# Performance work log

Hardware: AMD Instinct MI355X
Metric: run time of the kernel (lower is better)

Reference implementation:

```python
import jax, jax.numpy as jnp
import numpy as np

# Model dims (match init_kwargs): dim=768, num_heads=12, num_kv_heads=2 -> G=6, head_dim=64
DIM, HKV, G, D = 768, 2, 6, 64


def setup_inputs() -> dict:
    key = jax.random.key(0)
    ks = jax.random.split(key, 9)
    w = 0.02  # init scale for weights
    return {
        "x": jax.random.normal(ks[0], (8, 1024, DIM), dtype=jnp.float32),
        "depth_k": jax.random.normal(ks[1], (8, 1024, HKV, D), dtype=jnp.float32),
        "depth_v": jax.random.normal(ks[2], (8, 1024, HKV, D), dtype=jnp.float32),
        "Wq": jax.random.normal(ks[3], (DIM, DIM), dtype=jnp.float32) * w,
        "bq": jnp.zeros((DIM,), dtype=jnp.float32),
        "Wkv": jax.random.normal(ks[4], (2 * HKV * D, DIM), dtype=jnp.float32) * w,
        "bkv": jnp.zeros((2 * HKV * D,), dtype=jnp.float32),
        "Wproj": jax.random.normal(ks[5], (DIM, DIM), dtype=jnp.float32) * w,
        "bproj": jnp.zeros((DIM,), dtype=jnp.float32),
    }


def reference(x, depth_k, depth_v, Wq, bq, Wkv, bkv, Wproj, bproj):
    B, N, C = x.shape
    scale = D ** -0.5
    # Q projection, GQA groups unfolded into the sequence dim: [B, N*G, Hkv, D]
    q = (x @ Wq.T + bq).reshape(B, N * G, HKV, D)
    # KV projection: [B, N, 2, Hkv, D]
    kv = (x @ Wkv.T + bkv).reshape(B, N, 2, HKV, D)
    k, v = kv[:, :, 0], kv[:, :, 1]
    # Concatenate depth (previous-layer) KV cache along the sequence dim
    k_full = jnp.concatenate([depth_k, k], axis=1)  # [B, N_cache+N, Hkv, D]
    v_full = jnp.concatenate([depth_v, v], axis=1)
    # Full (non-causal) attention per kv head over the unfolded query sequence
    scores = jnp.einsum('bqhd,bkhd->bhqk', q, k_full) * scale  # [B, Hkv, N*G, Kv]
    attn = jax.nn.softmax(scores, axis=-1)
    o = jnp.einsum('bhqk,bkhd->bqhd', attn, v_full)  # [B, N*G, Hkv, D]
    out = o.reshape(B, N, C) @ Wproj.T + bproj  # fold G*Hkv*D back to C=dim
    return out, k, v
```

## Files before the change

### kernel.cpp

```cpp
#include <hip/hip_runtime.h>

using sh8 = __attribute__((ext_vector_type(8))) short;
using sh4 = __attribute__((ext_vector_type(4))) short;
using fx4 = __attribute__((ext_vector_type(4))) float;

#define MFMA(a,b,c)   __builtin_amdgcn_mfma_f32_16x16x32_bf16((a),(b),(c),0,0,0)

__device__ __forceinline__ short f2bf(float f) {
    union { float f; unsigned u; } v; v.f = f;
    return (short)((v.u + 0x7fffu + ((v.u >> 16) & 1u)) >> 16);
}

__device__ __forceinline__ unsigned cvtpk(float lo, float hi) {
    unsigned r;
    asm("v_cvt_pk_bf16_f32 %0, %1, %2" : "=v"(r) : "v"(lo), "v"(hi));
    return r;
}

__device__ __forceinline__ sh8 pack8(float4 a, float4 b) {
    union { unsigned u[4]; sh8 s; } r;
    r.u[0] = cvtpk(a.x, a.y);
    r.u[1] = cvtpk(a.z, a.w);
    r.u[2] = cvtpk(b.x, b.y);
    r.u[3] = cvtpk(b.z, b.w);
    return r.s;
}

#define QSCALE 0.18033688011112042f

#define GLOAD_LDS16(gsrc, ldst) __builtin_amdgcn_global_load_lds( \
    (const __attribute__((address_space(1))) void*)(gsrc),        \
    (__attribute__((address_space(3))) void*)(ldst), 16, 0, 0)

__global__ __launch_bounds__(256) void cast_k(const float* __restrict__ x,
                                              const float* __restrict__ Wq,
                                              const float* __restrict__ Wkv,
                                              short* __restrict__ xbf,
                                              short* __restrict__ wqbf,
                                              short* __restrict__ wkvbf)
{
    const int blk = blockIdx.x, t = threadIdx.x;
    const float* src; short* dst; size_t idx8;
    if (blk < 3072)      { src = x;   dst = xbf;   idx8 = ((size_t)blk * 256 + t) * 8; }
    else if (blk < 3360) { src = Wq;  dst = wqbf;  idx8 = ((size_t)(blk - 3072) * 256 + t) * 8; }
    else                 { src = Wkv; dst = wkvbf; idx8 = ((size_t)(blk - 3360) * 256 + t) * 8; }
    float4 a = *(const float4*)(src + idx8);
    float4 b = *(const float4*)(src + idx8 + 4);
    *(sh8*)&dst[idx8] = pack8(a, b);
}

__global__ __launch_bounds__(256) void wpcast_k(const float* __restrict__ Wp,
                                                short* __restrict__ wpbf)
{
    const size_t idx8 = ((size_t)blockIdx.x * 256 + threadIdx.x) * 8;
    float4 a = *(const float4*)(Wp + idx8);
    float4 b = *(const float4*)(Wp + idx8 + 4);
    *(sh8*)&wpbf[idx8] = pack8(a, b);
}


__global__ __launch_bounds__(256) void prep_k(const short* __restrict__ xbf,
                                              const short* __restrict__ wqbf,
                                              const short* __restrict__ wkvbf,
                                              const float* __restrict__ bq,
                                              const float* __restrict__ bkv,
                                              const float* __restrict__ dk,
                                              const float* __restrict__ dv,
                                              float* __restrict__ ok,
                                              float* __restrict__ ov,
                                              short* __restrict__ q_ws,
                                              short* __restrict__ k_ws,
                                              short* __restrict__ vT_ws)
{
    __shared__ alignas(16) short L[4][16][512];
    const int blk = blockIdx.x;
    const int t   = threadIdx.x;

    if (blk < 512) {
        const int x8 = blk & 7, jj = blk >> 3;
        const int m  = x8 * 8 + (jj >> 3);
        const int nn = jj & 7;
        const bool isq = (nn < 6);
        const int  bm  = m * 128, bn = (isq ? nn : nn - 6) * 128;
        const short* Wmat = isq ? wqbf : wkvbf;

        const int wave = t >> 6, lane = t & 63;
        const int wm   = wave >> 1, wn = wave & 1;
        const int lhi  = lane >> 4, llo = lane & 15;
        const int l15  = lane & 15, l4 = lane >> 4;

        const short* aSrc0 = xbf  + (size_t)(bm + wave*16     + l15)*768 + l4*8;
        const short* aSrc1 = xbf  + (size_t)(bm + (wave+4)*16 + l15)*768 + l4*8;
        const short* bSrc0 = Wmat + (size_t)(bn + wave*16     + l15)*768 + l4*8;
        const short* bSrc1 = Wmat + (size_t)(bn + (wave+4)*16 + l15)*768 + l4*8;

        auto stage = [&](int s) {
            const int r = s & 3;
            GLOAD_LDS16(aSrc0 + s*32, &L[r][wave][0]);
            GLOAD_LDS16(aSrc1 + s*32, &L[r][4 + wave][0]);
            GLOAD_LDS16(bSrc0 + s*32, &L[r][8 + wave][0]);
            GLOAD_LDS16(bSrc1 + s*32, &L[r][12 + wave][0]);
        };

        fx4 zero = {0.f, 0.f, 0.f, 0.f};
        fx4 acc[4][4];
        #pragma unroll
        for (int a = 0; a < 4; ++a)
            #pragma unroll
            for (int b2 = 0; b2 < 4; ++b2) acc[a][b2] = zero;

        stage(0);
        stage(1);

        for (int s = 0; s < 24; ++s) {
            if (s < 22) {
                stage(s + 2);
                asm volatile("s_waitcnt vmcnt(8)" ::: "memory");
            } else if (s == 22) {
                asm volatile("s_waitcnt vmcnt(4)" ::: "memory");
            } else {
                asm volatile("s_waitcnt vmcnt(0)" ::: "memory");
            }
            __builtin_amdgcn_s_barrier();
            __builtin_amdgcn_sched_barrier(0);

            const short* Lb = (const short*)&L[s & 3][0][0];
            const int lo = lane * 8;
            sh8 af[4], bf[4];
            #pragma unroll
            for (int mt = 0; mt < 4; ++mt)
                af[mt] = *(const sh8*)(Lb + (wm*4 + mt)*512 + lo);
            #pragma unroll
            for (int nt = 0; nt < 4; ++nt)
                bf[nt] = *(const sh8*)(Lb + (8 + wn*4 + nt)*512 + lo);
            #pragma unroll
            for (int mt = 0; mt < 4; ++mt)
                #pragma unroll
                for (int nt = 0; nt < 4; ++nt)
                    acc[mt][nt] = MFMA(af[mt], bf[nt], acc[mt][nt]);
        }

        if (isq) {
            #pragma unroll
            for (int nt = 0; nt < 4; ++nt) {
                const int c = bn + wn*64 + nt*16 + llo;
                const float bias = bq[c];
                const int g = c >> 7, h = (c >> 6) & 1, d = c & 63;
                #pragma unroll
                for (int mt = 0; mt < 4; ++mt) {
                    const int m0 = bm + wm*64 + mt*16 + lhi*4;
                    #pragma unroll
                    for (int r = 0; r < 4; ++r) {
                        const int mr = m0 + r;
                        const int b = mr >> 10, n = mr & 1023;
                        const float val = (acc[mt][nt][r] + bias) * QSCALE;
                        q_ws[((size_t)(b*2 + h)*6144 + n*6 + g)*64 + d] = f2bf(val);
                    }
                }
            }
        } else {
            #pragma unroll
            for (int nt = 0; nt < 4; ++nt) {
                const int c = bn + wn*64 + nt*16 + llo;
                const float bias = bkv[c];
                const int s = c >> 7, h = (c >> 6) & 1, d = c & 63;
                #pragma unroll
                for (int mt = 0; mt < 4; ++mt) {
                    const int m0 = bm + wm*64 + mt*16 + lhi*4;
                    const int b = m0 >> 10, n0 = m0 & 1023;
                    float vals[4];
                    #pragma unroll
                    for (int r = 0; r < 4; ++r) vals[r] = acc[mt][nt][r] + bias;
                    const int key = 1024 + n0;
                    if (s == 0) {
                        #pragma unroll
                        for (int r = 0; r < 4; ++r)
                            ok[((size_t)(b*1024 + n0 + r)*2 + h)*64 + d] = vals[r];
                        const int kb_ = key >> 6, nt_ = (key >> 4) & 3;
                        const int half = d >> 5, lhiK = (d >> 3) & 3, jK = d & 7;
                        const size_t base = (size_t)(b*2 + h)*131072
                            + (size_t)(((((kb_*4 + nt_)*2 + half)*64) + lhiK*16 + (key & 15))*8 + jK);
                        #pragma unroll
                        for (int r = 0; r < 4; ++r)
                            k_ws[base + r*8] = f2bf(vals[r]);
                    } else {
                        #pragma unroll
                        for (int r = 0; r < 4; ++r)
                            ov[((size_t)(b*1024 + n0 + r)*2 + h)*64 + d] = vals[r];
                        const int kb_ = key >> 6, g_ = (key >> 5) & 1, k5 = key & 31;
                        const int half5 = k5 >> 4, lhi5 = (k5 >> 2) & 3;
                        const int dt_ = d >> 4, llov = d & 15;
                        short4 pk = make_short4(f2bf(vals[0]), f2bf(vals[1]),
                                                f2bf(vals[2]), f2bf(vals[3]));
                        const size_t base = (size_t)(b*2 + h)*131072
                            + (size_t)(((((kb_*2 + g_)*4 + dt_)*64) + lhi5*16 + llov)*8 + half5*4);
                        *(short4*)&vT_ws[base] = pk;
                    }
                }
            }
        }
    } else if (blk < 1536) {
        const size_t idx4 = ((size_t)(blk - 512) * 256 + t) * 4;
        const int b  = (int)(idx4 >> 17);
        const int rm = (int)(idx4 & 131071);
        const int tt = rm >> 7, h = (rm >> 6) & 1, d = rm & 63;
        float4 v = *(const float4*)(dk + idx4);
        short4 pk = make_short4(f2bf(v.x), f2bf(v.y), f2bf(v.z), f2bf(v.w));
        const int kb_ = tt >> 6, nt_ = (tt >> 4) & 3, lloK = tt & 15;
        const int half = d >> 5, lhiK = (d >> 3) & 3, jK = d & 7;
        const size_t addr = (size_t)(b*2 + h)*131072
            + (size_t)(((((kb_*4 + nt_)*2 + half)*64) + lhiK*16 + lloK)*8 + jK);
        *(short4*)&k_ws[addr] = pk;
    } else {
        const int unit = (blk - 1536)*4 + (t >> 6);
        const int lane = t & 63, lhi = lane >> 4, llo = lane & 15;
        const int dt_ = unit & 3, g_ = (unit >> 2) & 1;
        const int kb_ = (unit >> 3) & 15, bh = unit >> 7;
        const int b = bh >> 1, h = bh & 1;
        const float* s0 = dv
            + ((size_t)((b*1024 + kb_*64 + g_*32 + lhi*4)*2 + h))*64 + dt_*16 + llo;
        union { short s[8]; sh8 v8; } o;
        #pragma unroll
        for (int jv = 0; jv < 4; ++jv) o.s[jv]     = f2bf(s0[(size_t)jv * 128]);
        #pragma unroll
        for (int jv = 0; jv < 4; ++jv) o.s[4 + jv] = f2bf(s0[(size_t)(16 + jv) * 128]);
        *(sh8*)&vT_ws[((size_t)bh*256 + (kb_*2 + g_)*4 + dt_)*512 + lane*8] = o.v8;
    }
}

__global__ __launch_bounds__(256) void attn_k(const short* __restrict__ q_ws,
                                              const short* __restrict__ k_ws,
                                              const short* __restrict__ vT_ws,
                                              short* __restrict__ o_ws)
{
    __shared__ alignas(16) short L[4][8][512];
    const int t    = threadIdx.x;
    const int wave = t >> 6, lane = t & 63;
    const int lhi  = lane >> 4, llo = lane & 15;
    const int blk  = blockIdx.x;
    const int x8   = blk & 7, jj = blk >> 3;
    const int bh   = x8 * 2 + (jj >= 48 ? 1 : 0);
    const int qt   = (jj >= 48) ? (jj - 48) : jj;
    const int b    = bh >> 1, h = bh & 1;

    const short* qb = q_ws + ((size_t)bh*6144 + qt*128 + wave*32) * 64;
    sh8 qf[2][2];
    #pragma unroll
    for (int s = 0; s < 2; ++s) {
        qf[s][0] = *(const sh8*)(qb + (s*16 + llo)*64 + lhi*8);
        qf[s][1] = *(const sh8*)(qb + (s*16 + llo)*64 + lhi*8 + 32);
    }

    const short* kbase = k_ws  + (size_t)bh*131072;
    const short* vbase = vT_ws + (size_t)bh*131072;

    fx4 zero = {0.f, 0.f, 0.f, 0.f};
    fx4 oacc[2][4];
    fx4 lacc[2];
    #pragma unroll
    for (int s = 0; s < 2; ++s) {
        lacc[s] = zero;
        #pragma unroll
        for (int dt = 0; dt < 4; ++dt) oacc[s][dt] = zero;
    }

    union { unsigned u[4]; sh8 s8; } onesu;
    onesu.u[0] = onesu.u[1] = onesu.u[2] = onesu.u[3] = 0x3F803F80u;
    const sh8 ones = onesu.s8;

    auto stage = [&](int g) {
        const short* ks = kbase + ((size_t)g*4 + wave)*512 + lane*8;
        const short* vs = vbase + ((size_t)g*4 + wave)*512 + lane*8;
        GLOAD_LDS16(ks, &L[g & 3][wave][0]);
        GLOAD_LDS16(vs, &L[g & 3][4 + wave][0]);
    };

    stage(0);
    stage(1);

    for (int g = 0; g < 64; ++g) {
        if (g < 62) {
            stage(g + 2);
            asm volatile("s_waitcnt vmcnt(4)" ::: "memory");
        } else if (g == 62) {
            asm volatile("s_waitcnt vmcnt(2)" ::: "memory");
        } else {
            asm volatile("s_waitcnt vmcnt(0)" ::: "memory");
        }
        __builtin_amdgcn_s_barrier();
        __builtin_amdgcn_sched_barrier(0);

        const short* Lb = (const short*)&L[g & 3][0][0];
        const int lo = lane * 8;
        sh8 K0 = *(const sh8*)(Lb + lo);
        sh8 K1 = *(const sh8*)(Lb + 512  + lo);
        sh8 K2 = *(const sh8*)(Lb + 1024 + lo);
        sh8 K3 = *(const sh8*)(Lb + 1536 + lo);
        sh8 V0 = *(const sh8*)(Lb + 2048 + lo);
        sh8 V1 = *(const sh8*)(Lb + 2560 + lo);
        sh8 V2 = *(const sh8*)(Lb + 3072 + lo);
        sh8 V3 = *(const sh8*)(Lb + 3584 + lo);

        #pragma unroll
        for (int s = 0; s < 2; ++s) {
            fx4 stA = MFMA(K0, qf[s][0], zero); stA = MFMA(K1, qf[s][1], stA);
            fx4 stB = MFMA(K2, qf[s][0], zero); stB = MFMA(K3, qf[s][1], stB);
            float pa0 = __builtin_amdgcn_exp2f(stA[0]);
            float pa1 = __builtin_amdgcn_exp2f(stA[1]);
            float pa2 = __builtin_amdgcn_exp2f(stA[2]);
            float pa3 = __builtin_amdgcn_exp2f(stA[3]);
            float pb0 = __builtin_amdgcn_exp2f(stB[0]);
            float pb1 = __builtin_amdgcn_exp2f(stB[1]);
            float pb2 = __builtin_amdgcn_exp2f(stB[2]);
            float pb3 = __builtin_amdgcn_exp2f(stB[3]);
            union { unsigned u[4]; sh8 s8; } pu;
            pu.u[0] = cvtpk(pa0, pa1);
            pu.u[1] = cvtpk(pa2, pa3);
            pu.u[2] = cvtpk(pb0, pb1);
            pu.u[3] = cvtpk(pb2, pb3);
            lacc[s]    = MFMA(pu.s8, ones, lacc[s]);
            oacc[s][0] = MFMA(pu.s8, V0, oacc[s][0]);
            oacc[s][1] = MFMA(pu.s8, V1, oacc[s][1]);
            oacc[s][2] = MFMA(pu.s8, V2, oacc[s][2]);
            oacc[s][3] = MFMA(pu.s8, V3, oacc[s][3]);
        }
    }

    #pragma unroll
    for (int s = 0; s < 2; ++s) {
        #pragma unroll
        for (int r = 0; r < 4; ++r) {
            const float iq = 1.0f / lacc[s][r];
            const int qi = qt*128 + wave*32 + s*16 + lhi*4 + r;
            const int n = qi / 6, g = qi % 6;
            short* orow = o_ws + ((size_t)(b*1024 + n))*768 + g*128 + h*64;
            #pragma unroll
            for (int dt = 0; dt < 4; ++dt)
                orow[dt*16 + llo] = f2bf(oacc[s][dt][r] * iq);
        }
    }
}

__global__ __launch_bounds__(256) void projgemm_k(const short* __restrict__ o_ws,
                                                  const short* __restrict__ wpbf,
                                                  const float* __restrict__ bpj,
                                                  float* __restrict__ out)
{
    __shared__ alignas(16) short L[4][12][512];
    const int t    = threadIdx.x;
    const int wave = t >> 6, lane = t & 63;
    const int wm   = wave >> 1, wn = wave & 1;
    const int lhi  = lane >> 4, llo = lane & 15;
    const int l15  = lane & 15, l4 = lane >> 4;
    const int x8   = blockIdx.x & 7, jj = blockIdx.x >> 3;
    const int bm   = (x8*8 + jj/12) * 128;
    const int bn   = (jj % 12) * 64;

    const short* aSrc0 = o_ws + (size_t)(bm + wave*16     + l15)*768 + l4*8;
    const short* aSrc1 = o_ws + (size_t)(bm + (wave+4)*16 + l15)*768 + l4*8;
    const short* bSrc  = wpbf + (size_t)(bn + wave*16     + l15)*768 + l4*8;

    auto stage = [&](int s) {
        const int r = s & 3;
        GLOAD_LDS16(aSrc0 + s*32, &L[r][wave][0]);
        GLOAD_LDS16(aSrc1 + s*32, &L[r][4 + wave][0]);
        GLOAD_LDS16(bSrc  + s*32, &L[r][8 + wave][0]);
    };

    fx4 zero = {0.f, 0.f, 0.f, 0.f};
    fx4 acc[4][2];
    #pragma unroll
    for (int i = 0; i < 4; ++i)
        #pragma unroll
        for (int j2 = 0; j2 < 2; ++j2) acc[i][j2] = zero;

    stage(0);
    stage(1);

    for (int s = 0; s < 24; ++s) {
        if (s < 22) {
            stage(s + 2);
            asm volatile("s_waitcnt vmcnt(6)" ::: "memory");
        } else if (s == 22) {
            asm volatile("s_waitcnt vmcnt(3)" ::: "memory");
        } else {
            asm volatile("s_waitcnt vmcnt(0)" ::: "memory");
        }
        __builtin_amdgcn_s_barrier();
        __builtin_amdgcn_sched_barrier(0);

        const short* Lb = (const short*)&L[s & 3][0][0];
        const int lo = lane * 8;
        sh8 af[4], bf[2];
        #pragma unroll
        for (int mt = 0; mt < 4; ++mt)
            af[mt] = *(const sh8*)(Lb + (wm*4 + mt)*512 + lo);
        #pragma unroll
        for (int nt = 0; nt < 2; ++nt)
            bf[nt] = *(const sh8*)(Lb + (8 + wn*2 + nt)*512 + lo);
        #pragma unroll
        for (int mt = 0; mt < 4; ++mt)
            #pragma unroll
            for (int nt = 0; nt < 2; ++nt)
                acc[mt][nt] = MFMA(af[mt], bf[nt], acc[mt][nt]);
    }

    #pragma unroll
    for (int nt = 0; nt < 2; ++nt) {
        const int c = bn + wn*32 + nt*16 + llo;
        const float bias = bpj[c];
        #pragma unroll
        for (int mt = 0; mt < 4; ++mt) {
            const int m0 = bm + wm*64 + mt*16 + lhi*4;
            #pragma unroll
            for (int r = 0; r < 4; ++r)
                out[(size_t)(m0 + r)*768 + c] = acc[mt][nt][r] + bias;
        }
    }
}

extern "C" void kernel_launch(void* const* d_in, const int* in_sizes, int n_in,
                              void* d_out, int out_size, void* d_ws, size_t ws_size,
                              hipStream_t stream)
{
    const float* x   = (const float*)d_in[0];
    const float* dk  = (const float*)d_in[1];
    const float* dv  = (const float*)d_in[2];
    const float* Wq  = (const float*)d_in[3];
    const float* bq  = (const float*)d_in[4];
    const float* Wkv = (const float*)d_in[5];
    const float* bkv = (const float*)d_in[6];
    const float* Wp  = (const float*)d_in[7];
    const float* bpj = (const float*)d_in[8];

    float* out = (float*)d_out;
    float* ok  = out + 6291456;
    float* ov  = out + 7340032;

    short* xbf   = (short*)out;
    short* wqbf  = xbf + 6291456;
    short* wkvbf = wqbf + 589824;

    char* ws = (char*)d_ws;
    short* q_ws  = (short*)(ws);
    short* k_ws  = (short*)(ws + 12582912);
    short* vT_ws = (short*)(ws + 16777216);
    short* o_ws  = (short*)(ws + 20971520);

    short* wpbf  = q_ws;

    cast_k     <<<dim3(3456), 256, 0, stream>>>(x, Wq, Wkv, xbf, wqbf, wkvbf);
    prep_k     <<<dim3(2048), 256, 0, stream>>>(xbf, wqbf, wkvbf, bq, bkv, dk, dv,
                                                ok, ov, q_ws, k_ws, vT_ws);
    attn_k     <<<dim3(768),  256, 0, stream>>>(q_ws, k_ws, vT_ws, o_ws);
    wpcast_k   <<<dim3(288),  256, 0, stream>>>(Wp, wpbf);
    projgemm_k <<<dim3(768),  256, 0, stream>>>(o_ws, wpbf, bpj, out);
}
```

Before: 209.2 us.

## Give each attention wave private K/V staging and more query rows per block

Each wave now loads the whole K/V tile it needs into its own LDS region, so the per-iteration block barrier is gone, and the ring shrinks from four to two stages. Each wave handles 48 query rows instead of 32, so the grid drops from 768 to 512 blocks and each loaded K/V tile serves more queries. The PV MFMAs also get a raised wave priority via s_setprio. The trade-offs are four times the K/V global traffic per block, since every wave loads the full tile, along with higher register use, LDS doubling to 64KB, and fewer blocks for load balancing.

```diff
diff --git a/kernel.cpp b/kernel.cpp
--- a/kernel.cpp
+++ b/kernel.cpp
@@ -233,32 +233,46 @@
                                               const short* __restrict__ vT_ws,
                                               short* __restrict__ o_ws)
 {
-    __shared__ alignas(16) short L[4][8][512];
+    __shared__ alignas(16) short L[2][4][8][512];
     const int t    = threadIdx.x;
     const int wave = t >> 6, lane = t & 63;
     const int lhi  = lane >> 4, llo = lane & 15;
     const int blk  = blockIdx.x;
     const int x8   = blk & 7, jj = blk >> 3;
-    const int bh   = x8 * 2 + (jj >= 48 ? 1 : 0);
-    const int qt   = (jj >= 48) ? (jj - 48) : jj;
+    const int bh   = x8 * 2 + (jj >= 32 ? 1 : 0);
+    const int qt   = (jj >= 32) ? (jj - 32) : jj;
     const int b    = bh >> 1, h = bh & 1;
 
-    const short* qb = q_ws + ((size_t)bh*6144 + qt*128 + wave*32) * 64;
-    sh8 qf[2][2];
+    const short* qb = q_ws + ((size_t)bh*6144 + qt*192 + wave*48) * 64;
+    sh8 qf[3][2];
     #pragma unroll
-    for (int s = 0; s < 2; ++s) {
+    for (int s = 0; s < 3; ++s) {
         qf[s][0] = *(const sh8*)(qb + (s*16 + llo)*64 + lhi*8);
         qf[s][1] = *(const sh8*)(qb + (s*16 + llo)*64 + lhi*8 + 32);
     }
 
-    const short* kbase = k_ws  + (size_t)bh*131072;
-    const short* vbase = vT_ws + (size_t)bh*131072;
+    const short* kb_ = k_ws  + (size_t)bh*131072 + lane*8;
+    const short* vb_ = vT_ws + (size_t)bh*131072 + lane*8;
+
+    auto stage = [&](int g) {
+        const short* ks = kb_ + (size_t)g * 2048;
+        const short* vs = vb_ + (size_t)g * 2048;
+        short* dst = &L[g & 1][wave][0][0];
+        GLOAD_LDS16(ks,        dst);
+        GLOAD_LDS16(ks + 512,  dst + 512);
+        GLOAD_LDS16(ks + 1024, dst + 1024);
+        GLOAD_LDS16(ks + 1536, dst + 1536);
+        GLOAD_LDS16(vs,        dst + 2048);
+        GLOAD_LDS16(vs + 512,  dst + 2560);
+        GLOAD_LDS16(vs + 1024, dst + 3072);
+        GLOAD_LDS16(vs + 1536, dst + 3584);
+    };
 
     fx4 zero = {0.f, 0.f, 0.f, 0.f};
-    fx4 oacc[2][4];
-    fx4 lacc[2];
+    fx4 oacc[3][4];
+    fx4 lacc[3];
     #pragma unroll
-    for (int s = 0; s < 2; ++s) {
+    for (int s = 0; s < 3; ++s) {
         lacc[s] = zero;
         #pragma unroll
         for (int dt = 0; dt < 4; ++dt) oacc[s][dt] = zero;
@@ -268,29 +282,18 @@
     onesu.u[0] = onesu.u[1] = onesu.u[2] = onesu.u[3] = 0x3F803F80u;
     const sh8 ones = onesu.s8;
 
-    auto stage = [&](int g) {
-        const short* ks = kbase + ((size_t)g*4 + wave)*512 + lane*8;
-        const short* vs = vbase + ((size_t)g*4 + wave)*512 + lane*8;
-        GLOAD_LDS16(ks, &L[g & 3][wave][0]);
-        GLOAD_LDS16(vs, &L[g & 3][4 + wave][0]);
-    };
-
     stage(0);
-    stage(1);
 
     for (int g = 0; g < 64; ++g) {
-        if (g < 62) {
-            stage(g + 2);
-            asm volatile("s_waitcnt vmcnt(4)" ::: "memory");
-        } else if (g == 62) {
-            asm volatile("s_waitcnt vmcnt(2)" ::: "memory");
+        if (g < 63) {
+            stage(g + 1);
+            asm volatile("s_waitcnt vmcnt(8)" ::: "memory");
         } else {
             asm volatile("s_waitcnt vmcnt(0)" ::: "memory");
         }
-        __builtin_amdgcn_s_barrier();
         __builtin_amdgcn_sched_barrier(0);
 
-        const short* Lb = (const short*)&L[g & 3][0][0];
+        const short* Lb = (const short*)&L[g & 1][wave][0][0];
         const int lo = lane * 8;
         sh8 K0 = *(const sh8*)(Lb + lo);
         sh8 K1 = *(const sh8*)(Lb + 512  + lo);
@@ -302,7 +305,7 @@
         sh8 V3 = *(const sh8*)(Lb + 3584 + lo);
 
         #pragma unroll
-        for (int s = 0; s < 2; ++s) {
+        for (int s = 0; s < 3; ++s) {
             fx4 stA = MFMA(K0, qf[s][0], zero); stA = MFMA(K1, qf[s][1], stA);
             fx4 stB = MFMA(K2, qf[s][0], zero); stB = MFMA(K3, qf[s][1], stB);
             float pa0 = __builtin_amdgcn_exp2f(stA[0]);
@@ -318,22 +321,24 @@
             pu.u[1] = cvtpk(pa2, pa3);
             pu.u[2] = cvtpk(pb0, pb1);
             pu.u[3] = cvtpk(pb2, pb3);
+            __builtin_amdgcn_s_setprio(1);
             lacc[s]    = MFMA(pu.s8, ones, lacc[s]);
             oacc[s][0] = MFMA(pu.s8, V0, oacc[s][0]);
             oacc[s][1] = MFMA(pu.s8, V1, oacc[s][1]);
             oacc[s][2] = MFMA(pu.s8, V2, oacc[s][2]);
             oacc[s][3] = MFMA(pu.s8, V3, oacc[s][3]);
+            __builtin_amdgcn_s_setprio(0);
         }
     }
 
     #pragma unroll
-    for (int s = 0; s < 2; ++s) {
+    for (int s = 0; s < 3; ++s) {
         #pragma unroll
         for (int r = 0; r < 4; ++r) {
             const float iq = 1.0f / lacc[s][r];
-            const int qi = qt*128 + wave*32 + s*16 + lhi*4 + r;
-            const int n = qi / 6, g = qi % 6;
-            short* orow = o_ws + ((size_t)(b*1024 + n))*768 + g*128 + h*64;
+            const int qi = qt*192 + wave*48 + s*16 + lhi*4 + r;
+            const int n = qi / 6, g6 = qi % 6;
+            short* orow = o_ws + ((size_t)(b*1024 + n))*768 + g6*128 + h*64;
             #pragma unroll
             for (int dt = 0; dt < 4; ++dt)
                 orow[dt*16 + llo] = f2bf(oacc[s][dt][r] * iq);
@@ -452,7 +457,7 @@
     cast_k     <<<dim3(3456), 256, 0, stream>>>(x, Wq, Wkv, xbf, wqbf, wkvbf);
     prep_k     <<<dim3(2048), 256, 0, stream>>>(xbf, wqbf, wkvbf, bq, bkv, dk, dv,
                                                 ok, ov, q_ws, k_ws, vT_ws);
-    attn_k     <<<dim3(768),  256, 0, stream>>>(q_ws, k_ws, vT_ws, o_ws);
+    attn_k     <<<dim3(512),  256, 0, stream>>>(q_ws, k_ws, vT_ws, o_ws);
     wpcast_k   <<<dim3(288),  256, 0, stream>>>(Wp, wpbf);
     projgemm_k <<<dim3(768),  256, 0, stream>>>(o_ws, wpbf, bpj, out);
 }
```

Measured after the change: 222.2 us. 6.3% more time.

## Software-pipeline attention loop: overlap next tile QK MFMAs with current exp/PV

Applied to the files above, without the earlier changes.

Restructures the attention inner loop so that the QK^T score MFMAs for tile g+1 are issued while tile g's scores go through exp2, bf16 packing and the PV/row-sum MFMAs. Scores and V fragments are carried across iterations in registers, with a prologue and an epilogue. The global-to-LDS prefetch depth also grows from two to three tiles in flight, using the four-slot ring buffer. This is meant to hide the transcendental and convert latency behind matrix work and to cover more load latency, at the cost of extra live registers for the carried scores and V, which may lower occupancy.

```diff
diff --git a/kernel.cpp b/kernel.cpp
--- a/kernel.cpp
+++ b/kernel.cpp
@@ -275,54 +275,117 @@
         GLOAD_LDS16(vs, &L[g & 3][4 + wave][0]);
     };
 
+    const int lo = lane * 8;
+    fx4 stc[2][2];
+    sh8 V0, V1, V2, V3;
+
     stage(0);
     stage(1);
-
-    for (int g = 0; g < 64; ++g) {
-        if (g < 62) {
-            stage(g + 2);
-            asm volatile("s_waitcnt vmcnt(4)" ::: "memory");
-        } else if (g == 62) {
-            asm volatile("s_waitcnt vmcnt(2)" ::: "memory");
-        } else {
-            asm volatile("s_waitcnt vmcnt(0)" ::: "memory");
-        }
-        __builtin_amdgcn_s_barrier();
-        __builtin_amdgcn_sched_barrier(0);
-
-        const short* Lb = (const short*)&L[g & 3][0][0];
-        const int lo = lane * 8;
+    stage(2);
+    asm volatile("s_waitcnt vmcnt(4)" ::: "memory");
+    __builtin_amdgcn_s_barrier();
+    __builtin_amdgcn_sched_barrier(0);
+    {
+        const short* Lb = (const short*)&L[0][0][0];
         sh8 K0 = *(const sh8*)(Lb + lo);
         sh8 K1 = *(const sh8*)(Lb + 512  + lo);
         sh8 K2 = *(const sh8*)(Lb + 1024 + lo);
         sh8 K3 = *(const sh8*)(Lb + 1536 + lo);
-        sh8 V0 = *(const sh8*)(Lb + 2048 + lo);
-        sh8 V1 = *(const sh8*)(Lb + 2560 + lo);
-        sh8 V2 = *(const sh8*)(Lb + 3072 + lo);
-        sh8 V3 = *(const sh8*)(Lb + 3584 + lo);
-
+        V0 = *(const sh8*)(Lb + 2048 + lo);
+        V1 = *(const sh8*)(Lb + 2560 + lo);
+        V2 = *(const sh8*)(Lb + 3072 + lo);
+        V3 = *(const sh8*)(Lb + 3584 + lo);
         #pragma unroll
         for (int s = 0; s < 2; ++s) {
-            fx4 stA = MFMA(K0, qf[s][0], zero); stA = MFMA(K1, qf[s][1], stA);
-            fx4 stB = MFMA(K2, qf[s][0], zero); stB = MFMA(K3, qf[s][1], stB);
-            float pa0 = __builtin_amdgcn_exp2f(stA[0]);
-            float pa1 = __builtin_amdgcn_exp2f(stA[1]);
-            float pa2 = __builtin_amdgcn_exp2f(stA[2]);
-            float pa3 = __builtin_amdgcn_exp2f(stA[3]);
-            float pb0 = __builtin_amdgcn_exp2f(stB[0]);
-            float pb1 = __builtin_amdgcn_exp2f(stB[1]);
-            float pb2 = __builtin_amdgcn_exp2f(stB[2]);
-            float pb3 = __builtin_amdgcn_exp2f(stB[3]);
-            union { unsigned u[4]; sh8 s8; } pu;
-            pu.u[0] = cvtpk(pa0, pa1);
-            pu.u[1] = cvtpk(pa2, pa3);
-            pu.u[2] = cvtpk(pb0, pb1);
-            pu.u[3] = cvtpk(pb2, pb3);
-            lacc[s]    = MFMA(pu.s8, ones, lacc[s]);
-            oacc[s][0] = MFMA(pu.s8, V0, oacc[s][0]);
-            oacc[s][1] = MFMA(pu.s8, V1, oacc[s][1]);
-            oacc[s][2] = MFMA(pu.s8, V2, oacc[s][2]);
-            oacc[s][3] = MFMA(pu.s8, V3, oacc[s][3]);
+            stc[s][0] = MFMA(K0, qf[s][0], zero); stc[s][0] = MFMA(K1, qf[s][1], stc[s][0]);
+            stc[s][1] = MFMA(K2, qf[s][0], zero); stc[s][1] = MFMA(K3, qf[s][1], stc[s][1]);
+        }
+    }
+
+    for (int g = 0; g < 63; ++g) {
+        if (g < 61) {
+            stage(g + 3);
+            asm volatile("s_waitcnt vmcnt(4)" ::: "memory");
+        } else if (g == 61) {
+            asm volatile("s_waitcnt vmcnt(2)" ::: "memory");
+        } else {
+            asm volatile("s_waitcnt vmcnt(0)" ::: "memory");
+        }
+        __builtin_amdgcn_s_barrier();
+        __builtin_amdgcn_sched_barrier(0);
+
+        const short* Lb = (const short*)&L[(g + 1) & 3][0][0];
+        sh8 K0 = *(const sh8*)(Lb + lo);
+        sh8 K1 = *(const sh8*)(Lb + 512  + lo);
+        sh8 K2 = *(const sh8*)(Lb + 1024 + lo);
+        sh8 K3 = *(const sh8*)(Lb + 1536 + lo);
+        sh8 Vn0 = *(const sh8*)(Lb + 2048 + lo);
+        sh8 Vn1 = *(const sh8*)(Lb + 2560 + lo);
+        sh8 Vn2 = *(const sh8*)(Lb + 3072 + lo);
+        sh8 Vn3 = *(const sh8*)(Lb + 3584 + lo);
+
+        union { unsigned u[4]; sh8 s8; } pu[2];
+        #pragma unroll
+        for (int s = 0; s < 2; ++s) {
+            float pa0 = __builtin_amdgcn_exp2f(stc[s][0][0]);
+            float pa1 = __builtin_amdgcn_exp2f(stc[s][0][1]);
+            float pa2 = __builtin_amdgcn_exp2f(stc[s][0][2]);
+            float pa3 = __builtin_amdgcn_exp2f(stc[s][0][3]);
+            float pb0 = __builtin_amdgcn_exp2f(stc[s][1][0]);
+            float pb1 = __builtin_amdgcn_exp2f(stc[s][1][1]);
+            float pb2 = __builtin_amdgcn_exp2f(stc[s][1][2]);
+            float pb3 = __builtin_amdgcn_exp2f(stc[s][1][3]);
+            pu[s].u[0] = cvtpk(pa0, pa1);
+            pu[s].u[1] = cvtpk(pa2, pa3);
+            pu[s].u[2] = cvtpk(pb0, pb1);
+            pu[s].u[3] = cvtpk(pb2, pb3);
+        }
+
+        fx4 stn[2][2];
+        #pragma unroll
+        for (int s = 0; s < 2; ++s) {
+            stn[s][0] = MFMA(K0, qf[s][0], zero); stn[s][0] = MFMA(K1, qf[s][1], stn[s][0]);
+            stn[s][1] = MFMA(K2, qf[s][0], zero); stn[s][1] = MFMA(K3, qf[s][1], stn[s][1]);
+        }
+
+        #pragma unroll
+        for (int s = 0; s < 2; ++s) {
+            lacc[s]    = MFMA(pu[s].s8, ones, lacc[s]);
+            oacc[s][0] = MFMA(pu[s].s8, V0, oacc[s][0]);
+            oacc[s][1] = MFMA(pu[s].s8, V1, oacc[s][1]);
+            oacc[s][2] = MFMA(pu[s].s8, V2, oacc[s][2]);
+            oacc[s][3] = MFMA(pu[s].s8, V3, oacc[s][3]);
+        }
+
+        #pragma unroll
+        for (int s = 0; s < 2; ++s) { stc[s][0] = stn[s][0]; stc[s][1] = stn[s][1]; }
+        V0 = Vn0; V1 = Vn1; V2 = Vn2; V3 = Vn3;
+    }
+
+    {
+        union { unsigned u[4]; sh8 s8; } pu[2];
+        #pragma unroll
+        for (int s = 0; s < 2; ++s) {
+            float pa0 = __builtin_amdgcn_exp2f(stc[s][0][0]);
+            float pa1 = __builtin_amdgcn_exp2f(stc[s][0][1]);
+            float pa2 = __builtin_amdgcn_exp2f(stc[s][0][2]);
+            float pa3 = __builtin_amdgcn_exp2f(stc[s][0][3]);
+            float pb0 = __builtin_amdgcn_exp2f(stc[s][1][0]);
+            float pb1 = __builtin_amdgcn_exp2f(stc[s][1][1]);
+            float pb2 = __builtin_amdgcn_exp2f(stc[s][1][2]);
+            float pb3 = __builtin_amdgcn_exp2f(stc[s][1][3]);
+            pu[s].u[0] = cvtpk(pa0, pa1);
+            pu[s].u[1] = cvtpk(pa2, pa3);
+            pu[s].u[2] = cvtpk(pb0, pb1);
+            pu[s].u[3] = cvtpk(pb2, pb3);
+        }
+        #pragma unroll
+        for (int s = 0; s < 2; ++s) {
+            lacc[s]    = MFMA(pu[s].s8, ones, lacc[s]);
+            oacc[s][0] = MFMA(pu[s].s8, V0, oacc[s][0]);
+            oacc[s][1] = MFMA(pu[s].s8, V1, oacc[s][1]);
+            oacc[s][2] = MFMA(pu[s].s8, V2, oacc[s][2]);
+            oacc[s][3] = MFMA(pu[s].s8, V3, oacc[s][3]);
         }
     }
 
@@ -332,8 +395,8 @@
         for (int r = 0; r < 4; ++r) {
             const float iq = 1.0f / lacc[s][r];
             const int qi = qt*128 + wave*32 + s*16 + lhi*4 + r;
-            const int n = qi / 6, g = qi % 6;
-            short* orow = o_ws + ((size_t)(b*1024 + n))*768 + g*128 + h*64;
+            const int n = qi / 6, g6 = qi % 6;
+            short* orow = o_ws + ((size_t)(b*1024 + n))*768 + g6*128 + h*64;
             #pragma unroll
             for (int dt = 0; dt < 4; ++dt)
                 orow[dt*16 + llo] = f2bf(oacc[s][dt][r] * iq);
```

Result: slower. 216.0 us (+3.3%).
